# Kernel optimization log

Hardware: AMD Instinct MI355X
Metric: run time of the kernel (lower is better)

## Reference

```python
import jax, jax.numpy as jnp
import numpy as np

NH = 4       # n_heads
R = 3        # n_rounds
LN_EPS = 1e-5
NEG = -1e9   # large negative for masked attention (avoids NaN on fully-masked rows)


def _mha(q, k, v, w, b, block=None):
    # w: [4, D, D] = (Wq, Wk, Wv, Wo); b: [4, D]. batch_first MHA, no dropout (eval).
    B, Nq, Dm = q.shape
    hd = Dm // NH

    def proj(x, wi, bi):
        return (x @ wi + bi).reshape(B, -1, NH, hd).transpose(0, 2, 1, 3)  # [B,h,N,hd]

    Q = proj(q, w[0], b[0])
    K = proj(k, w[1], b[1])
    V = proj(v, w[2], b[2])
    s = jnp.einsum('bhqd,bhkd->bhqk', Q, K) * (1.0 / np.sqrt(hd))
    if block is not None:  # block[b,q,k]=True means masked out
        s = jnp.where(block[:, None, :, :], NEG, s)
    p = jax.nn.softmax(s, axis=-1)
    o = jnp.einsum('bhqk,bhkd->bhqd', p, V).transpose(0, 2, 1, 3).reshape(B, -1, Dm)
    return o @ w[3] + b[3]


def setup_inputs() -> dict:
    key = jax.random.key(0)
    ks = jax.random.split(key, 16)
    B, N, Dm = 256, 128, 256
    s = 0.02
    return {
        'H': jax.random.normal(ks[0], (B, N, Dm), jnp.float32),
        'pred_heads': jax.random.randint(ks[1], (B, N), 0, N),
        'mask': jnp.ones((B, N), jnp.float32),
        'ha_w': jax.random.normal(ks[2], (R, 4, Dm, Dm)) * s,
        'ha_b': jnp.zeros((R, 4, Dm)),
        'sa_w': jax.random.normal(ks[3], (R, 4, Dm, Dm)) * s,
        'sa_b': jnp.zeros((R, 4, Dm)),
        'ct_w': jax.random.normal(ks[4], (R, 2 * Dm, Dm)) * s,
        'ct_b': jnp.zeros((R, Dm)),
        'gate_w': jax.random.normal(ks[5], (R, 4 * Dm, Dm)) * s,
        'gate_b': jnp.zeros((R, Dm)),
        'tr_w': jax.random.normal(ks[6], (R, 4 * Dm, Dm)) * s,
        'tr_b': jnp.zeros((R, Dm)),
        'ln_g': jnp.ones((R, Dm)),
        'ln_b': jnp.zeros((R, Dm)),
        'arc_head_w': jax.random.normal(ks[7], (Dm, Dm)) * s,
        'arc_head_b': jnp.zeros((Dm,)),
        'arc_dep_w': jax.random.normal(ks[8], (Dm, Dm)) * s,
        'arc_dep_b': jnp.zeros((Dm,)),
        'bilinear': jax.random.normal(ks[9], (Dm, Dm)) * np.sqrt(2.0 / Dm).astype(np.float32),
        'bh_w': jax.random.normal(ks[10], (Dm,)) * s,
        'bh_b': jnp.zeros(()),
        'bd_w': jax.random.normal(ks[11], (Dm,)) * s,
        'bd_b': jnp.zeros(()),
    }


def reference(H, pred_heads, mask, ha_w, ha_b, sa_w, sa_b, ct_w, ct_b,
              gate_w, gate_b, tr_w, tr_b, ln_g, ln_b,
              arc_head_w, arc_head_b, arc_dep_w, arc_dep_b, bilinear,
              bh_w, bh_b, bd_w, bd_b):
    B, N, Dm = H.shape
    mb = mask > 0
    hi = jnp.clip(pred_heads, 0, N - 1)
    hi3 = jnp.broadcast_to(hi[:, :, None], (B, N, Dm))
    bidx = jnp.arange(B)[:, None]
    eye = jnp.eye(N, dtype=bool)
    # sibling mask: same predicted head, not self, both positions valid (constant across rounds)
    sib = (pred_heads[:, :, None] == pred_heads[:, None, :]) & ~eye[None] \
          & mb[:, None, :] & mb[:, :, None]
    block = ~sib

    Hr = H
    for i in range(R):
        # gather head representation, attend to it
        head_repr = jnp.take_along_axis(Hr, hi3, axis=1)
        head_msg = _mha(Hr, head_repr, head_repr, ha_w[i], ha_b[i])
        # scatter-add children onto their heads, average
        child_sum = jnp.zeros_like(Hr).at[bidx, hi].add(Hr)
        child_count = jnp.zeros((B, N), Hr.dtype).at[bidx, hi].add(mask)
        child_avg = child_sum / jnp.maximum(child_count, 1.0)[:, :, None]
        child_msg = jax.nn.gelu(
            jnp.concatenate([Hr, child_avg], -1) @ ct_w[i] + ct_b[i], approximate=False)
        # masked sibling self-attention (N <= 128 branch)
        sib_msg = _mha(Hr, Hr, Hr, sa_w[i], sa_b[i], block=block)
        # gated fuse + residual + LayerNorm
        comb = jnp.concatenate([Hr, head_msg, child_msg, sib_msg], -1)
        g = jax.nn.sigmoid(comb @ gate_w[i] + gate_b[i])
        u = jax.nn.gelu(comb @ tr_w[i] + tr_b[i], approximate=False)
        Hn = Hr + g * u
        mu = Hn.mean(-1, keepdims=True)
        var = ((Hn - mu) ** 2).mean(-1, keepdims=True)
        Hr = (Hn - mu) / jnp.sqrt(var + LN_EPS) * ln_g[i] + ln_b[i]

    h_head = Hr @ arc_head_w + arc_head_b
    h_dep = Hr @ arc_dep_w + arc_dep_b
    scores = jnp.einsum('bnd,de,bme->bnm', h_head, bilinear, h_dep)
    scores = scores + (h_head @ bh_w + bh_b)[:, None, :] + (h_dep @ bd_w + bd_b)[:, :, None]
    return Hr, scores
```

## Files before the change

### kernel.cpp

```cpp
#include <hip/hip_runtime.h>
#include <hip/hip_bf16.h>
#include <math.h>

typedef __hip_bfloat16 bf16;
typedef __attribute__((ext_vector_type(8))) short bf16x8v;
typedef __attribute__((ext_vector_type(4))) float f32x4v;

#define BD 256
#define NN 128
#define DM 256
#define NHD 4
#define HDIM 64
#define RR 3

__device__ __forceinline__ float b2f(bf16 x) { return __bfloat162float(x); }
__device__ __forceinline__ bf16 f2b(float x) { return __float2bfloat16(x); }
__device__ __forceinline__ float geluf(float x) { return 0.5f * x * (1.f + erff(x * 0.70710678118654752f)); }

#define GLOAD16(g, l) __builtin_amdgcn_global_load_lds( \
    (const __attribute__((address_space(1))) void*)(g), \
    (__attribute__((address_space(3))) void*)(l), 16, 0, 0)

__global__ __launch_bounds__(256) void cvt32to16_kernel(
    const float* __restrict__ in, bf16* __restrict__ out, int n)
{
  int i = blockIdx.x * 256 + threadIdx.x;
  int stride = gridDim.x * 256;
  for (; i < n; i += stride) out[i] = f2b(in[i]);
}

__global__ __launch_bounds__(256) void cvt16to32_kernel(
    const bf16* __restrict__ in, float* __restrict__ out, int n)
{
  int i = blockIdx.x * 256 + threadIdx.x;
  int stride = gridDim.x * 256;
  for (; i < n; i += stride) out[i] = b2f(in[i]);
}

struct TDesc { const float* src; bf16* dst; int K; int base; };
struct TTable { TDesc e[12]; };

__global__ __launch_bounds__(256) void transpose_w_kernel(TTable T, int nent)
{
  int t = blockIdx.x;
  int ei = 0;
  for (int i = 1; i < nent; i++) if (t >= T.e[i].base) ei = i;
  const float* src = T.e[ei].src;
  bf16* dst = T.e[ei].dst;
  int K = T.e[ei].K;
  int lt = t - T.e[ei].base;
  int nt = lt & 7, kt = lt >> 3;

  __shared__ float tile[32][33];
  int tx = threadIdx.x & 31, ty = threadIdx.x >> 5;
#pragma unroll
  for (int i = 0; i < 4; i++)
    tile[ty + i * 8][tx] = src[(size_t)(kt * 32 + ty + i * 8) * 256 + nt * 32 + tx];
  __syncthreads();
#pragma unroll
  for (int i = 0; i < 4; i++)
    dst[(size_t)(nt * 32 + ty + i * 8) * K + kt * 32 + tx] = f2b(tile[tx][ty + i * 8]);
}

struct FJob { const float* A; const float* B; bf16* outT; int koff; int kst; };
struct FJobs { FJob j[13]; };

__global__ __launch_bounds__(256) void wfuse_kernel(FJobs F)
{
  const FJob jb = F.j[blockIdx.y];
  const int k0 = blockIdx.x * 16;
  const int col = threadIdx.x;
  float acc[16];
#pragma unroll
  for (int i = 0; i < 16; i++) acc[i] = 0.f;
  for (int m = 0; m < 256; m++) {
    float bv = jb.B[(size_t)m * 256 + col];
#pragma unroll
    for (int i = 0; i < 16; i++)
      acc[i] += jb.A[(size_t)(k0 + i) * 256 + m] * bv;
  }
#pragma unroll
  for (int i = 0; i < 16; i++)
    jb.outT[(size_t)col * jb.kst + jb.koff + k0 + i] = f2b(acc[i]);
}

__global__ __launch_bounds__(256) void bfuse_kernel(
    const float* gate_w, const float* tr_w, const float* gate_b, const float* tr_b,
    const float* ha_b, const float* sa_b,
    const float* ahw, const float* ahb, const float* bil,
    const float* bhw, const float* bhb,
    float* fgb, float* ftb, float* fab_bias, float* vha, float* cha)
{
  int blk = blockIdx.x, col = threadIdx.x;
  if (blk < 6) {
    int r = blk >> 1; bool isT = blk & 1;
    const float* W  = (isT ? tr_w : gate_w) + (size_t)r * 262144;
    const float* b0 = (isT ? tr_b : gate_b) + (size_t)r * 256;
    const float* boh = ha_b + (size_t)r * 1024 + 768;
    const float* bos = sa_b + (size_t)r * 1024 + 768;
    float acc = b0[col];
    for (int m = 0; m < 256; m++) {
      acc += boh[m] * W[(size_t)(256 + m) * 256 + col];
      acc += bos[m] * W[(size_t)(768 + m) * 256 + col];
    }
    ((isT ? ftb : fgb) + (size_t)r * 256)[col] = acc;
  } else {
    float a1 = 0.f, a2 = 0.f;
    for (int m = 0; m < 256; m++) {
      a1 += ahb[m] * bil[(size_t)m * 256 + col];
      a2 += ahw[(size_t)col * 256 + m] * bhw[m];
    }
    fab_bias[col] = a1;
    vha[col] = a2;
    if (col == 0) {
      float c = bhb[0];
      for (int m = 0; m < 256; m++) c += ahb[m] * bhw[m];
      cha[0] = c;
    }
  }
}

struct ProjArgs {
  const bf16* Hc; const bf16* CA; const int* gather;
  const bf16* W[7];
  const float* bias[7];
  bf16* out[7];
};

__global__ __launch_bounds__(256) void proj_fused_kernel(ProjArgs P)
{
  const int b  = blockIdx.x & 255;
  const int nh = blockIdx.x >> 8;
  const int c0 = nh * 128;
  const int tid = threadIdx.x;
  const int w = tid >> 6;
  const int lane = tid & 63;
  const int wr = w >> 1, wc = w & 1;
  const int r16 = lane & 15;
  const int kg = lane >> 4;

  __shared__ __align__(16) char lds[81920];

  const char* Hb = (const char*)(P.Hc + (size_t)b * NN * DM);

#pragma unroll
  for (int i = 0; i < 16; i++) {
    int row = w * 32 + i * 2 + (lane >> 5);
    int src = row * 512 + (((lane & 31) * 16) ^ ((row & 7) << 4));
    GLOAD16(Hb + src, lds + w * 16384 + i * 1024);
  }

#define STAGE_W(WT, K2, KT, BUF) do { \
    _Pragma("unroll") \
    for (int i_ = 0; i_ < 2; i_++) { \
      int wrow_ = w * 32 + i_ * 16 + (lane >> 2); \
      int slot_ = (lane & 3) ^ ((wrow_ >> 1) & 3); \
      GLOAD16((const char*)(WT) + (size_t)(c0 + wrow_) * (K2) + (KT) * 64 + slot_ * 16, \
              lds + 65536 + (BUF) * 8192 + w * 2048 + i_ * 1024); \
    } } while (0)

  STAGE_W(P.W[0], 512, 0, 0);
  __syncthreads();

  int lrow[4], grow[4];
#pragma unroll
  for (int mi = 0; mi < 4; mi++) {
    lrow[mi] = wr * 64 + mi * 16 + r16;
    int g = P.gather[b * NN + lrow[mi]];
    grow[mi] = min(max(g, 0), NN - 1);
  }
  int wro[4];
#pragma unroll
  for (int ni = 0; ni < 4; ni++) {
    int ct_ = wc * 64 + ni * 16 + r16;
    wro[ni] = ct_ * 64 + ((kg ^ ((ct_ >> 1) & 3)) << 4);
  }

  const bf16* CAb = P.CA + (size_t)b * NN * DM;
  int buf = 0;
  f32x4v zero = {0.f, 0.f, 0.f, 0.f};

#pragma unroll
  for (int j = 0; j < 7; j++) {
    const bool GATH = (j == 1) || (j == 2);
    const bool TR   = (j == 2) || (j == 5);
    const bool ACT  = (j == 6);
    const int NKS = (j == 6) ? 16 : 8;
    const int K2  = (j == 6) ? 1024 : 512;
    const bf16* Wj  = P.W[j];
    const bf16* Wj1 = (j < 6) ? P.W[j + 1] : P.W[j];
    const int  K2n  = (j < 6) ? ((j + 1 == 6) ? 1024 : 512) : K2;

    f32x4v acc[4][4];
#pragma unroll
    for (int mi = 0; mi < 4; mi++)
#pragma unroll
      for (int ni = 0; ni < 4; ni++) acc[mi][ni] = zero;

    for (int kt = 0; kt < NKS; kt++) {
      if (!(j == 6 && kt + 1 == NKS)) {
        const bf16* Wn = (kt + 1 < NKS) ? Wj : Wj1;
        int nkt = (kt + 1 < NKS) ? kt + 1 : 0;
        int nK2 = (kt + 1 < NKS) ? K2 : K2n;
        STAGE_W(Wn, nK2, nkt, buf ^ 1);
      }

      bf16x8v a[4], wv[4];
      if (j == 6 && kt >= 8) {
#pragma unroll
        for (int mi = 0; mi < 4; mi++)
          a[mi] = *(const bf16x8v*)(CAb + (size_t)lrow[mi] * DM + (kt - 8) * 32 + kg * 8);
      } else {
#pragma unroll
        for (int mi = 0; mi < 4; mi++) {
          int ar = GATH ? grow[mi] : lrow[mi];
          int off = ar * 512 + (((kt * 64) + kg * 16) ^ ((ar & 7) << 4));
          a[mi] = *(const bf16x8v*)(lds + off);
        }
      }
#pragma unroll
      for (int ni = 0; ni < 4; ni++)
        wv[ni] = *(const bf16x8v*)(lds + 65536 + buf * 8192 + wro[ni]);

#pragma unroll
      for (int mi = 0; mi < 4; mi++)
#pragma unroll
        for (int ni = 0; ni < 4; ni++)
          acc[mi][ni] = __builtin_amdgcn_mfma_f32_16x16x32_bf16(a[mi], wv[ni], acc[mi][ni], 0, 0, 0);

      __syncthreads();
      buf ^= 1;
    }

    bf16* outj = P.out[j];
    const float* bj = P.bias[j];
#pragma unroll
    for (int ni = 0; ni < 4; ni++) {
      int col = c0 + wc * 64 + ni * 16 + r16;
      float bv = bj ? bj[col] : 0.f;
#pragma unroll
      for (int mi = 0; mi < 4; mi++) {
        int row0 = wr * 64 + mi * 16 + kg * 4;
        if (!TR) {
          size_t base = ((size_t)b * NN + row0) * DM + col;
#pragma unroll
          for (int r = 0; r < 4; r++) {
            float x = acc[mi][ni][r] + bv;
            if (ACT) x = geluf(x);
            outj[base + (size_t)r * DM] = f2b(x);
          }
        } else {
          size_t base = ((size_t)b * DM + col) * NN + row0;
#pragma unroll
          for (int r = 0; r < 4; r++)
            outj[base + r] = f2b(acc[mi][ni][r] + bv);
        }
      }
    }
  }
#undef STAGE_W
}

struct DJob {
  const bf16 *a0, *a1, *a2, *a3;
  const bf16 *W0, *W1;
  const float *b0, *b1;
  bf16 *o0, *o1;
  int K;
};

__global__ __launch_bounds__(512) void dualw_gemm_kernel(DJob jb)
{
  const int b  = blockIdx.x & 255;
  const int nh = blockIdx.x >> 8;
  const int c0 = nh * 128;
  const int tid = threadIdx.x;
  const int w = tid >> 6;
  const int jj = w >> 2;
  const int wsub = w & 3;
  const int wr = wsub >> 1, wc = wsub & 1;
  const int lane = tid & 63;
  const int r16 = lane & 15;
  const int kg = lane >> 4;
  const int K = jb.K;
  const int nk = K >> 5;

  __shared__ __align__(16) char lds[49152];

  const int srow = tid >> 2;
  const int skc  = tid & 3;
  const int sl   = skc ^ ((srow >> 1) & 3);
  const size_t aoff = ((size_t)b * NN + srow) * DM + sl * 8;
  const bf16* w0src = jb.W0 + (size_t)(c0 + srow) * K + sl * 8;
  const bf16* w1src = jb.W1 + (size_t)(c0 + srow) * K + sl * 8;
  const int wbase = w * 1024;

  f32x4v zero = {0.f, 0.f, 0.f, 0.f};
  f32x4v acc[4][4];
#pragma unroll
  for (int mi = 0; mi < 4; mi++)
#pragma unroll
    for (int ni = 0; ni < 4; ni++) acc[mi][ni] = zero;

  int a_ro[4], w_ro[4];
#pragma unroll
  for (int mi = 0; mi < 4; mi++) {
    int row = wr * 64 + mi * 16 + r16;
    a_ro[mi] = row * 64 + ((kg ^ ((row >> 1) & 3)) << 4);
  }
  const int wsel = 16384 + jj * 16384;
#pragma unroll
  for (int ni = 0; ni < 4; ni++) {
    int col = wc * 64 + ni * 16 + r16;
    w_ro[ni] = col * 64 + ((kg ^ ((col >> 1) & 3)) << 4);
  }

  {
    GLOAD16(jb.a0 + aoff, lds + wbase);
    GLOAD16(w0src,        lds + 16384 + wbase);
    GLOAD16(w1src,        lds + 32768 + wbase);
  }
  __syncthreads();

  int cur = 0;
  for (int kt = 0; kt < nk; kt++) {
    if (kt + 1 < nk) {
      int k0 = (kt + 1) << 5;
      int sg = k0 >> 8;
      const bf16* Ab = (sg == 0) ? jb.a0 : ((sg == 1) ? jb.a1 : ((sg == 2) ? jb.a2 : jb.a3));
      int ko = k0 & 255;
      int nb = (cur ^ 1) * 8192;
      GLOAD16(Ab + aoff + ko,  lds + nb + wbase);
      GLOAD16(w0src + k0,      lds + 16384 + nb + wbase);
      GLOAD16(w1src + k0,      lds + 32768 + nb + wbase);
    }

    const char* La = lds + cur * 8192;
    const char* Lw = lds + wsel + cur * 8192;
    bf16x8v a[4], ww[4];
#pragma unroll
    for (int mi = 0; mi < 4; mi++) a[mi] = *(const bf16x8v*)(La + a_ro[mi]);
#pragma unroll
    for (int ni = 0; ni < 4; ni++) ww[ni] = *(const bf16x8v*)(Lw + w_ro[ni]);
#pragma unroll
    for (int mi = 0; mi < 4; mi++)
#pragma unroll
      for (int ni = 0; ni < 4; ni++)
        acc[mi][ni] = __builtin_amdgcn_mfma_f32_16x16x32_bf16(a[mi], ww[ni], acc[mi][ni], 0, 0, 0);

    __syncthreads();
    cur ^= 1;
  }

  bf16* out = jj ? jb.o1 : jb.o0;
  const float* bias = jj ? jb.b1 : jb.b0;
#pragma unroll
  for (int ni = 0; ni < 4; ni++) {
    int col = c0 + wc * 64 + ni * 16 + r16;
    float bv = bias ? bias[col] : 0.f;
#pragma unroll
    for (int mi = 0; mi < 4; mi++) {
      int row0 = wr * 64 + mi * 16 + kg * 4;
      size_t base = ((size_t)b * NN + row0) * DM + col;
#pragma unroll
      for (int r = 0; r < 4; r++)
        out[base + (size_t)r * DM] = f2b(acc[mi][ni][r] + bv);
    }
  }
}

struct AttnArgs {
  const bf16 *Qa, *Ka, *Va; bf16* Oa;
  const bf16 *Qs, *Ks, *Vs; bf16* Os;
};

__global__ __launch_bounds__(256) void attn2_kernel(
    AttnArgs A, const int* __restrict__ ph, const float* __restrict__ mask)
{
  const int b = blockIdx.y, h = blockIdx.x;
  const bool has_mask = (blockIdx.z == 1);
  const bf16* Qb = has_mask ? A.Qs : A.Qa;
  const bf16* Kb = has_mask ? A.Ks : A.Ka;
  const bf16* Vt = has_mask ? A.Vs : A.Va;
  bf16* Ob       = has_mask ? A.Os : A.Oa;

  const int w = threadIdx.x >> 6;
  const int lane = threadIdx.x & 63;
  const int r16 = lane & 15, kg = lane >> 4;
  const int q0 = w * 32;

  __shared__ bf16 P_lds[4][32 * 128];
  __shared__ int   ph_sh[NN];
  __shared__ float mk_sh[NN];

  if (has_mask && threadIdx.x < NN) {
    ph_sh[threadIdx.x] = ph[(size_t)b * NN + threadIdx.x];
    mk_sh[threadIdx.x] = mask[(size_t)b * NN + threadIdx.x];
  }
  __syncthreads();

  const bf16* Qh = Qb + (size_t)b * NN * DM + (size_t)h * HDIM;
  const bf16* Kh = Kb + (size_t)b * NN * DM + (size_t)h * HDIM;
  const bf16* Vh = Vt + ((size_t)b * DM + (size_t)h * HDIM) * NN;

  f32x4v zero = {0.f, 0.f, 0.f, 0.f};

  f32x4v accs[2][8];
#pragma unroll
  for (int mi = 0; mi < 2; mi++)
#pragma unroll
    for (int ni = 0; ni < 8; ni++) accs[mi][ni] = zero;

#pragma unroll
  for (int ks = 0; ks < 2; ks++) {
    int d = ks * 32 + kg * 8;
    bf16x8v a[2], bb[8];
#pragma unroll
    for (int mi = 0; mi < 2; mi++)
      a[mi] = *(const bf16x8v*)(Qh + (size_t)(q0 + mi * 16 + r16) * DM + d);
#pragma unroll
    for (int ni = 0; ni < 8; ni++)
      bb[ni] = *(const bf16x8v*)(Kh + (size_t)(ni * 16 + r16) * DM + d);
#pragma unroll
    for (int mi = 0; mi < 2; mi++)
#pragma unroll
      for (int ni = 0; ni < 8; ni++)
        accs[mi][ni] = __builtin_amdgcn_mfma_f32_16x16x32_bf16(a[mi], bb[ni], accs[mi][ni], 0, 0, 0);
  }

#pragma unroll
  for (int mi = 0; mi < 2; mi++) {
#pragma unroll
    for (int r = 0; r < 4; r++) {
      int wq = mi * 16 + kg * 4 + r;
      int q_e = q0 + wq;
      float v[8];
      float mx = -3.0e38f;
      int qp = 0; float qm = 1.f;
      if (has_mask) { qp = ph_sh[q_e]; qm = mk_sh[q_e]; }
#pragma unroll
      for (int ni = 0; ni < 8; ni++) {
        float s = accs[mi][ni][r] * 0.125f;
        if (has_mask) {
          int t_e = ni * 16 + r16;
          bool sib = (qp == ph_sh[t_e]) && (q_e != t_e) && (qm > 0.f) && (mk_sh[t_e] > 0.f);
          if (!sib) s = -1e9f;
        }
        v[ni] = s;
        mx = fmaxf(mx, s);
      }
#pragma unroll
      for (int o = 1; o < 16; o <<= 1) mx = fmaxf(mx, __shfl_xor(mx, o, 64));
      float sum = 0.f;
#pragma unroll
      for (int ni = 0; ni < 8; ni++) { v[ni] = __expf(v[ni] - mx); sum += v[ni]; }
#pragma unroll
      for (int o = 1; o < 16; o <<= 1) sum += __shfl_xor(sum, o, 64);
      float inv = 1.f / sum;
      int swz = (wq & 7) << 3;
#pragma unroll
      for (int ni = 0; ni < 8; ni++) {
        int t_e = ni * 16 + r16;
        P_lds[w][(wq * 128 + t_e) ^ swz] = f2b(v[ni] * inv);
      }
    }
  }
  __syncthreads();

  f32x4v acco[2][4];
#pragma unroll
  for (int mi = 0; mi < 2; mi++)
#pragma unroll
    for (int ni = 0; ni < 4; ni++) acco[mi][ni] = zero;

#pragma unroll
  for (int kt = 0; kt < 4; kt++) {
    int t = kt * 32 + kg * 8;
    bf16x8v a[2], bb[4];
#pragma unroll
    for (int mi = 0; mi < 2; mi++) {
      int wqr = mi * 16 + r16;
      int idx = (wqr * 128 + t) ^ ((wqr & 7) << 3);
      a[mi] = *(const bf16x8v*)&P_lds[w][idx];
    }
#pragma unroll
    for (int ni = 0; ni < 4; ni++)
      bb[ni] = *(const bf16x8v*)(Vh + (size_t)(ni * 16 + r16) * NN + t);
#pragma unroll
    for (int mi = 0; mi < 2; mi++)
#pragma unroll
      for (int ni = 0; ni < 4; ni++)
        acco[mi][ni] = __builtin_amdgcn_mfma_f32_16x16x32_bf16(a[mi], bb[ni], acco[mi][ni], 0, 0, 0);
  }

#pragma unroll
  for (int ni = 0; ni < 4; ni++) {
    int d = ni * 16 + r16;
#pragma unroll
    for (int mi = 0; mi < 2; mi++) {
      int qrow = q0 + mi * 16 + kg * 4;
      size_t base = ((size_t)b * NN + qrow) * DM + (size_t)h * HDIM + d;
#pragma unroll
      for (int r = 0; r < 4; r++)
        Ob[base + (size_t)r * DM] = f2b(acco[mi][ni][r]);
    }
  }
}

__global__ __launch_bounds__(256) void child_avg2_kernel(
    const bf16* __restrict__ Hr, const int* __restrict__ ph,
    const float* __restrict__ mask, bf16* __restrict__ CA)
{
  const int b = blockIdx.x;
  const int t = threadIdx.x;
  __shared__ int hi[NN];
  __shared__ float mk[NN];
  __shared__ int cnt[NN], off[NN], rnk[NN], lst[NN];
  __shared__ float cntf[NN];

  if (t < NN) {
    int g = ph[(size_t)b * NN + t];
    hi[t] = min(max(g, 0), NN - 1);
    mk[t] = mask[(size_t)b * NN + t];
  }
  __syncthreads();
  if (t < NN) {
    int c = 0, r = 0; float cf = 0.f;
    int me = hi[t];
    for (int j = 0; j < NN; j++) {
      int hj = hi[j];
      c  += (hj == t);
      cf += (hj == t) ? mk[j] : 0.f;
      r  += (j < t) && (hj == me);
    }
    cnt[t] = c; cntf[t] = cf; rnk[t] = r;
  }
  __syncthreads();
  if (t < NN) {
    int o = 0;
    for (int m = 0; m < t; m++) o += cnt[m];
    off[t] = o;
  }
  __syncthreads();
  if (t < NN) lst[off[hi[t]] + rnk[t]] = t;
  __syncthreads();

  const bf16* Hb = Hr + (size_t)b * NN * DM;
  bf16* Cb = CA + (size_t)b * NN * DM;
  const int d = t;
  for (int m = 0; m < NN; m++) {
    float s = 0.f;
    int o = off[m], c = cnt[m];
    for (int i = 0; i < c; i++)
      s += b2f(Hb[(size_t)lst[o + i] * DM + d]);
    Cb[(size_t)m * DM + d] = f2b(s / fmaxf(cntf[m], 1.f));
  }
}

__global__ __launch_bounds__(256) void ln_epi_kernel(
    const bf16* __restrict__ Hr, const bf16* __restrict__ Gp, const bf16* __restrict__ Up,
    const float* __restrict__ lg, const float* __restrict__ lb, bf16* __restrict__ Hout)
{
  const int b = blockIdx.y;
  const int m0 = blockIdx.x * 8;
  const int c = threadIdx.x;
  __shared__ float red[8];
  float lgv = lg[c], lbv = lb[c];
  int wv = c >> 6, ln = c & 63;
  for (int m = 0; m < 8; m++) {
    size_t idx = ((size_t)b * NN + m0 + m) * DM + c;
    float g = 1.f / (1.f + __expf(-b2f(Gp[idx])));
    float u = geluf(b2f(Up[idx]));
    float hn = b2f(Hr[idx]) + g * u;
    float s1 = hn, s2 = hn * hn;
#pragma unroll
    for (int o = 1; o < 64; o <<= 1) { s1 += __shfl_xor(s1, o, 64); s2 += __shfl_xor(s2, o, 64); }
    if (ln == 0) { red[wv] = s1; red[4 + wv] = s2; }
    __syncthreads();
    float sum = red[0] + red[1] + red[2] + red[3];
    float sq  = red[4] + red[5] + red[6] + red[7];
    float mu = sum * (1.f / DM);
    float var = sq * (1.f / DM) - mu * mu;
    float y = (hn - mu) * rsqrtf(var + 1e-5f) * lgv + lbv;
    Hout[idx] = f2b(y);
    __syncthreads();
  }
}

__global__ __launch_bounds__(256) void rhrd2_kernel(
    const bf16* __restrict__ Hc, const bf16* __restrict__ hd,
    const float* __restrict__ vha, const float* __restrict__ cha,
    const float* __restrict__ bdw, const float* __restrict__ bdb,
    float* __restrict__ rh, float* __restrict__ rd)
{
  int b = blockIdx.x;
  int t = threadIdx.x;
  int n = t & 127;
  bool isD = t >= 128;
  if (!isD) {
    const bf16* row = Hc + ((size_t)b * NN + n) * DM;
    float s = cha[0];
    for (int k = 0; k < DM; k++) s += b2f(row[k]) * vha[k];
    rh[(size_t)b * NN + n] = s;
  } else {
    const bf16* row = hd + ((size_t)b * NN + n) * DM;
    float s = bdb[0];
    for (int k = 0; k < DM; k++) s += b2f(row[k]) * bdw[k];
    rd[(size_t)b * NN + n] = s;
  }
}

__global__ __launch_bounds__(512) void scores_mfma_kernel(
    const bf16* __restrict__ tmp, const bf16* __restrict__ hd,
    const float* __restrict__ rh, const float* __restrict__ rd,
    float* __restrict__ out)
{
  const int b = blockIdx.x;
  const int w = threadIdx.x >> 6;
  const int lane = threadIdx.x & 63;
  const int wr = w >> 1, wc = w & 1;
  const int r16 = lane & 15;
  const int kg = lane >> 4;

  size_t qoff[2], moff[4];
#pragma unroll
  for (int mi = 0; mi < 2; mi++) qoff[mi] = ((size_t)b * NN + wr * 32 + mi * 16 + r16) * DM;
#pragma unroll
  for (int ni = 0; ni < 4; ni++) moff[ni] = ((size_t)b * NN + wc * 64 + ni * 16 + r16) * DM;

  f32x4v zero = {0.f, 0.f, 0.f, 0.f};
  f32x4v acc[2][4];
#pragma unroll
  for (int mi = 0; mi < 2; mi++)
#pragma unroll
    for (int ni = 0; ni < 4; ni++) acc[mi][ni] = zero;

  for (int k0 = 0; k0 < DM; k0 += 32) {
    int k = k0 + kg * 8;
    bf16x8v a[2], bb[4];
#pragma unroll
    for (int mi = 0; mi < 2; mi++) a[mi] = *(const bf16x8v*)(tmp + qoff[mi] + k);
#pragma unroll
    for (int ni = 0; ni < 4; ni++) bb[ni] = *(const bf16x8v*)(hd + moff[ni] + k);
#pragma unroll
    for (int mi = 0; mi < 2; mi++)
#pragma unroll
      for (int ni = 0; ni < 4; ni++)
        acc[mi][ni] = __builtin_amdgcn_mfma_f32_16x16x32_bf16(a[mi], bb[ni], acc[mi][ni], 0, 0, 0);
  }

#pragma unroll
  for (int ni = 0; ni < 4; ni++) {
    int m = wc * 64 + ni * 16 + r16;
    float rhm = rh[b * NN + m];
#pragma unroll
    for (int mi = 0; mi < 2; mi++) {
      int q0 = wr * 32 + mi * 16 + kg * 4;
#pragma unroll
      for (int r = 0; r < 4; r++)
        out[(size_t)b * NN * NN + (size_t)(q0 + r) * NN + m] =
            acc[mi][ni][r] + rhm + rd[b * NN + q0 + r];
    }
  }
}

extern "C" void kernel_launch(void* const* d_in, const int* in_sizes, int n_in,
                              void* d_out, int out_size, void* d_ws, size_t ws_size,
                              hipStream_t stream) {
  const float* H      = (const float*)d_in[0];
  const int*   ph     = (const int*)  d_in[1];
  const float* mask   = (const float*)d_in[2];
  const float* ha_w   = (const float*)d_in[3];
  const float* ha_b   = (const float*)d_in[4];
  const float* sa_w   = (const float*)d_in[5];
  const float* sa_b   = (const float*)d_in[6];
  const float* ct_w   = (const float*)d_in[7];
  const float* ct_b   = (const float*)d_in[8];
  const float* gate_w = (const float*)d_in[9];
  const float* gate_b = (const float*)d_in[10];
  const float* tr_w   = (const float*)d_in[11];
  const float* tr_b   = (const float*)d_in[12];
  const float* ln_g   = (const float*)d_in[13];
  const float* ln_b   = (const float*)d_in[14];
  const float* ahw    = (const float*)d_in[15];
  const float* ahb    = (const float*)d_in[16];
  const float* adw    = (const float*)d_in[17];
  const float* adb    = (const float*)d_in[18];
  const float* bil    = (const float*)d_in[19];
  const float* bhw    = (const float*)d_in[20];
  const float* bhb    = (const float*)d_in[21];
  const float* bdw    = (const float*)d_in[22];
  const float* bdb    = (const float*)d_in[23];

  const size_t AB = (size_t)BD * NN * DM;
  bf16* wsb  = (bf16*)d_ws;
  bf16* Hcur = wsb + 0 * AB;
  bf16* Qa   = wsb + 1 * AB;
  bf16* Ka   = wsb + 2 * AB;
  bf16* Va   = wsb + 3 * AB;
  bf16* Qs   = wsb + 4 * AB;
  bf16* Ks   = wsb + 5 * AB;
  bf16* Vs   = wsb + 6 * AB;
  bf16* mC   = wsb + 7 * AB;
  float* rh  = (float*)(wsb + 8 * AB);
  float* rd  = rh + (size_t)BD * NN;
  float* fgb = rd + (size_t)BD * NN;
  float* ftb = fgb + 768;
  float* fab_bias = ftb + 768;
  float* vha = fab_bias + 256;
  float* cha = vha + 256;

  bf16* D0 = (bf16*)d_out;
  bf16* D1 = D0 + AB;
  bf16* D2 = D0 + 2 * AB;
  const size_t RS = 1179648;
  bf16* adT  = D2 + 3 * RS;
  bf16* fabT = adT + 65536;

  cvt32to16_kernel<<<dim3(2048), 256, 0, stream>>>(H, Hcur, (int)AB);

  for (int r = 0; r < RR; r++) {
    bf16* base_r = D2 + (size_t)r * RS;
    bf16* haT = base_r;
    bf16* saT = base_r + 262144;
    bf16* ctT = base_r + 524288;
    bf16* gT  = base_r + 655360;
    bf16* tT  = base_r + 917504;
    TTable T; int base = 0;
    for (int i = 0; i < 3; i++) {
      T.e[i] = { ha_w + ((size_t)r * 4 + i) * 65536, haT + (size_t)i * 65536, 256, base };
      base += 64;
    }
    for (int i = 0; i < 3; i++) {
      T.e[3 + i] = { sa_w + ((size_t)r * 4 + i) * 65536, saT + (size_t)i * 65536, 256, base };
      base += 64;
    }
    T.e[6] = { ct_w + (size_t)r * 131072, ctT, 512, base };                    base += 128;
    T.e[7] = { gate_w + (size_t)r * 262144,             gT,        1024, base }; base += 64;
    T.e[8] = { gate_w + (size_t)r * 262144 + 512 * 256, gT + 512,  1024, base }; base += 64;
    T.e[9] = { tr_w   + (size_t)r * 262144,             tT,        1024, base }; base += 64;
    T.e[10]= { tr_w   + (size_t)r * 262144 + 512 * 256, tT + 512,  1024, base }; base += 64;
    int nent = 11;
    if (r == 0) { T.e[11] = { adw, adT, 256, base }; base += 64; nent = 12; }
    transpose_w_kernel<<<dim3(base), 256, 0, stream>>>(T, nent);
  }
  {
    FJobs F;
    for (int r = 0; r < RR; r++) {
      bf16* gT = D2 + (size_t)r * RS + 655360;
      bf16* tT = D2 + (size_t)r * RS + 917504;
      const float* WoH = ha_w + ((size_t)r * 4 + 3) * 65536;
      const float* WoS = sa_w + ((size_t)r * 4 + 3) * 65536;
      const float* gw = gate_w + (size_t)r * 262144;
      const float* tw = tr_w   + (size_t)r * 262144;
      F.j[r * 4 + 0] = { WoH, gw + 256 * 256, gT, 256, 1024 };
      F.j[r * 4 + 1] = { WoS, gw + 768 * 256, gT, 768, 1024 };
      F.j[r * 4 + 2] = { WoH, tw + 256 * 256, tT, 256, 1024 };
      F.j[r * 4 + 3] = { WoS, tw + 768 * 256, tT, 768, 1024 };
    }
    F.j[12] = { ahw, bil, fabT, 0, 256 };
    wfuse_kernel<<<dim3(16, 13), 256, 0, stream>>>(F);
  }
  bfuse_kernel<<<dim3(7), 256, 0, stream>>>(gate_w, tr_w, gate_b, tr_b,
      ha_b, sa_b, ahw, ahb, bil, bhw, bhb, fgb, ftb, fab_bias, vha, cha);

  for (int r = 0; r < RR; r++) {
    bf16* base_r = D2 + (size_t)r * RS;
    bf16* haT = base_r;
    bf16* saT = base_r + 262144;
    bf16* ctT = base_r + 524288;
    bf16* gT  = base_r + 655360;
    bf16* tT  = base_r + 917504;
    const float* hab = ha_b + (size_t)r * 4 * DM;
    const float* sab = sa_b + (size_t)r * 4 * DM;

    child_avg2_kernel<<<dim3(BD), 256, 0, stream>>>(Hcur, ph, mask, D0);

    {
      ProjArgs P;
      P.Hc = Hcur; P.CA = D0; P.gather = ph;
      P.W[0] = haT;          P.bias[0] = hab + 0;   P.out[0] = Qa;
      P.W[1] = haT + 65536;  P.bias[1] = hab + 256; P.out[1] = Ka;
      P.W[2] = haT + 131072; P.bias[2] = hab + 512; P.out[2] = Va;
      P.W[3] = saT;          P.bias[3] = sab + 0;   P.out[3] = Qs;
      P.W[4] = saT + 65536;  P.bias[4] = sab + 256; P.out[4] = Ks;
      P.W[5] = saT + 131072; P.bias[5] = sab + 512; P.out[5] = Vs;
      P.W[6] = ctT;          P.bias[6] = ct_b + (size_t)r * DM; P.out[6] = mC;
      proj_fused_kernel<<<dim3(512), 256, 0, stream>>>(P);
    }

    {
      AttnArgs A = { Qa, Ka, Va, D0, Qs, Ks, Vs, D1 };
      attn2_kernel<<<dim3(NHD, BD, 2), 256, 0, stream>>>(A, ph, mask);
    }

    {
      DJob J = { Hcur, D0, mC, D1, gT, tT,
                 fgb + (size_t)r * 256, ftb + (size_t)r * 256, Va, Vs, 1024 };
      dualw_gemm_kernel<<<dim3(512), 512, 0, stream>>>(J);
    }

    ln_epi_kernel<<<dim3(16, BD), 256, 0, stream>>>(Hcur, Va, Vs,
        ln_g + (size_t)r * DM, ln_b + (size_t)r * DM, Hcur);
  }

  {
    DJob J = { Hcur, Hcur, Hcur, Hcur, adT, fabT, adb, fab_bias, Ka, Va, 256 };
    dualw_gemm_kernel<<<dim3(512), 512, 0, stream>>>(J);
  }
  rhrd2_kernel<<<dim3(BD), 256, 0, stream>>>(Hcur, Ka, vha, cha, bdw, bdb, rh, rd);
  scores_mfma_kernel<<<dim3(BD), 512, 0, stream>>>(Va, Ka, rh, rd, (float*)d_out + AB);

  cvt16to32_kernel<<<dim3(2048), 256, 0, stream>>>(Hcur, (float*)d_out, (int)AB);
}
```

Before: 936.4 us.

## Use per-wave triple-buffered weight staging without block barriers in projection GEMM

In the fused projection kernel, each wave now stages its own 64 weight columns into a private LDS region with a three-deep ring buffer. Completion is tracked with explicit vmcnt waits instead of a block-wide __syncthreads after every k-step. Loads run two tiles ahead, including across the boundaries between the seven projections. The aim is to remove barrier stalls and hide global-to-LDS latency. The cost is duplicated weight fetches across row-waves and LDS growing from 80KB to 112KB, which may reduce blocks per CU.

```diff
diff --git a/kernel.cpp b/kernel.cpp
--- a/kernel.cpp
+++ b/kernel.cpp
@@ -139,7 +139,7 @@
   const int r16 = lane & 15;
   const int kg = lane >> 4;
 
-  __shared__ __align__(16) char lds[81920];
+  __shared__ __align__(16) char lds[114688];
 
   const char* Hb = (const char*)(P.Hc + (size_t)b * NN * DM);
 
@@ -150,16 +150,21 @@
     GLOAD16(Hb + src, lds + w * 16384 + i * 1024);
   }
 
-#define STAGE_W(WT, K2, KT, BUF) do { \
+  const int WB = 65536 + w * 12288;
+  const int wcol0 = c0 + wc * 64;
+
+#define ISSUE_W(WT, K2B, KTL, BUF) do { \
     _Pragma("unroll") \
-    for (int i_ = 0; i_ < 2; i_++) { \
-      int wrow_ = w * 32 + i_ * 16 + (lane >> 2); \
-      int slot_ = (lane & 3) ^ ((wrow_ >> 1) & 3); \
-      GLOAD16((const char*)(WT) + (size_t)(c0 + wrow_) * (K2) + (KT) * 64 + slot_ * 16, \
-              lds + 65536 + (BUF) * 8192 + w * 2048 + i_ * 1024); \
+    for (int i_ = 0; i_ < 4; i_++) { \
+      int lc_ = i_ * 16 + (lane >> 2); \
+      int sl_ = (lane & 3) ^ ((lc_ >> 1) & 3); \
+      GLOAD16((const char*)(WT) + (size_t)(wcol0 + lc_) * (K2B) + (KTL) * 64 + sl_ * 16, \
+              lds + WB + (BUF) * 4096 + i_ * 1024); \
     } } while (0)
 
-  STAGE_W(P.W[0], 512, 0, 0);
+  ISSUE_W(P.W[0], 512, 0, 0);
+  ISSUE_W(P.W[0], 512, 1, 1);
+  ISSUE_W(P.W[0], 512, 2, 2);
   __syncthreads();
 
   int lrow[4], grow[4];
@@ -172,8 +177,8 @@
   int wro[4];
 #pragma unroll
   for (int ni = 0; ni < 4; ni++) {
-    int ct_ = wc * 64 + ni * 16 + r16;
-    wro[ni] = ct_ * 64 + ((kg ^ ((ct_ >> 1) & 3)) << 4);
+    int lc = ni * 16 + r16;
+    wro[ni] = lc * 64 + ((kg ^ ((lc >> 1) & 3)) << 4);
   }
 
   const bf16* CAb = P.CA + (size_t)b * NN * DM;
@@ -186,10 +191,10 @@
     const bool TR   = (j == 2) || (j == 5);
     const bool ACT  = (j == 6);
     const int NKS = (j == 6) ? 16 : 8;
-    const int K2  = (j == 6) ? 1024 : 512;
+    const int K2B = (j == 6) ? 1024 : 512;
     const bf16* Wj  = P.W[j];
     const bf16* Wj1 = (j < 6) ? P.W[j + 1] : P.W[j];
-    const int  K2n  = (j < 6) ? ((j + 1 == 6) ? 1024 : 512) : K2;
+    const int  K2Bn = (j < 6) ? ((j + 1 == 6) ? 1024 : 512) : K2B;
 
     f32x4v acc[4][4];
 #pragma unroll
@@ -198,19 +203,16 @@
       for (int ni = 0; ni < 4; ni++) acc[mi][ni] = zero;
 
     for (int kt = 0; kt < NKS; kt++) {
-      if (!(j == 6 && kt + 1 == NKS)) {
-        const bf16* Wn = (kt + 1 < NKS) ? Wj : Wj1;
-        int nkt = (kt + 1 < NKS) ? kt + 1 : 0;
-        int nK2 = (kt + 1 < NKS) ? K2 : K2n;
-        STAGE_W(Wn, nK2, nkt, buf ^ 1);
-      }
-
       bf16x8v a[4], wv[4];
       if (j == 6 && kt >= 8) {
 #pragma unroll
         for (int mi = 0; mi < 4; mi++)
           a[mi] = *(const bf16x8v*)(CAb + (size_t)lrow[mi] * DM + (kt - 8) * 32 + kg * 8);
+        asm volatile("s_waitcnt vmcnt(0)" ::: "memory");
+        __builtin_amdgcn_sched_barrier(0);
       } else {
+        asm volatile("s_waitcnt vmcnt(8)" ::: "memory");
+        __builtin_amdgcn_sched_barrier(0);
 #pragma unroll
         for (int mi = 0; mi < 4; mi++) {
           int ar = GATH ? grow[mi] : lrow[mi];
@@ -220,7 +222,7 @@
       }
 #pragma unroll
       for (int ni = 0; ni < 4; ni++)
-        wv[ni] = *(const bf16x8v*)(lds + 65536 + buf * 8192 + wro[ni]);
+        wv[ni] = *(const bf16x8v*)(lds + WB + buf * 4096 + wro[ni]);
 
 #pragma unroll
       for (int mi = 0; mi < 4; mi++)
@@ -228,8 +230,15 @@
         for (int ni = 0; ni < 4; ni++)
           acc[mi][ni] = __builtin_amdgcn_mfma_f32_16x16x32_bf16(a[mi], wv[ni], acc[mi][ni], 0, 0, 0);
 
-      __syncthreads();
-      buf ^= 1;
+      __builtin_amdgcn_sched_barrier(0);
+
+      int nkt = kt + 3;
+      if (nkt < NKS) {
+        ISSUE_W(Wj, K2B, nkt, buf);
+      } else if (j < 6) {
+        ISSUE_W(Wj1, K2Bn, nkt - NKS, buf);
+      }
+      buf = (buf + 1) % 3;
     }
 
     bf16* outj = P.out[j];
@@ -258,7 +267,7 @@
       }
     }
   }
-#undef STAGE_W
+#undef ISSUE_W
 }
 
 struct DJob {
```

Result: slower. 1.035 ms (+10.5%).
